# Performance work log

Hardware: AMD Instinct MI355X
Metric: run time of the kernel (lower is better)

Reference implementation:

```python
import jax, jax.numpy as jnp
import numpy as np
from jax import lax

B, C, N = 8, 3, 65536
NUM_POINTS = 1024


def setup_inputs() -> dict:
    key = jax.random.key(0)
    points = jax.random.normal(key, (B, C, N), dtype=jnp.float32)
    return {"points": points}


def furthest_point_sampling(xyz, num_points):
    # xyz: (B, N, 3) -> indices (B, num_points), int32
    b, n, _ = xyz.shape
    init_idx = jnp.zeros((b,), dtype=jnp.int32)  # CUDA FPS seeds with index 0
    init_dists = jnp.full((b, n), 1e10, dtype=xyz.dtype)

    def step(carry, _):
        dists, last_idx = carry
        last_pt = jnp.take_along_axis(xyz, last_idx[:, None, None], axis=1)  # (B,1,3)
        d = jnp.sum(jnp.square(xyz - last_pt), axis=-1)  # (B,N) squared dist to newest pt
        dists = jnp.minimum(dists, d)
        nxt = jnp.argmax(dists, axis=-1).astype(jnp.int32)
        return (dists, nxt), nxt

    (_, _), rest = lax.scan(step, (init_dists, init_idx), None, length=num_points - 1)
    # rest: (num_points-1, B) -> (B, num_points)
    idx = jnp.concatenate([init_idx[None, :], rest], axis=0).T
    return idx


def reference(points):
    # points: (B, 3, N), channels-first as in the torch module
    xyz = jnp.transpose(points, (0, 2, 1))  # (B, N, 3)
    idx = furthest_point_sampling(xyz, NUM_POINTS)  # (B, num_points)
    # fps_gather_by_index: gather along point axis of (B, 3, N)
    new_points = jnp.take_along_axis(points, idx[:, None, :], axis=2)  # (B, 3, num_points)
    return new_points
```

## Files before the change

kernel.cpp:

```cpp
#include <hip/hip_runtime.h>


namespace {

constexpr int kB = 8;
constexpr int kN = 65536;
constexpr int kNP = 1024;
constexpr int kPB = 16;
constexpr int kThreads = 256;
constexpr int kPPT = kN / (kPB * kThreads);
constexpr int kGrp = kPPT / 4;
constexpr int kWaves = kThreads / 64;
constexpr int kRgn = 16;

__device__ __forceinline__ unsigned long long shfl_xor_u64(unsigned long long v, int off) {
  return (unsigned long long)__shfl_xor((long long)v, off, 64);
}

__device__ __forceinline__ unsigned long long u64max(unsigned long long a,
                                                     unsigned long long b) {
  return a > b ? a : b;
}

__device__ __forceinline__ unsigned long long load_l2(const unsigned long long* p) {
  unsigned long long v;
  asm volatile("global_load_dwordx2 %0, %1, off sc0\n\ts_waitcnt vmcnt(0)"
               : "=v"(v)
               : "v"(p)
               : "memory");
  return v;
}

__device__ __forceinline__ void store_l2(unsigned long long* p, unsigned long long v) {
  asm volatile("global_store_dwordx2 %0, %1, off sc0" ::"v"(p), "v"(v) : "memory");
}

__global__ __launch_bounds__(kThreads) void fps_kernel(const float* __restrict__ pts,
                                                       float* __restrict__ out,
                                                       unsigned long long* __restrict__ slots) {
  const int batch = blockIdx.x & 7;
  const int slice = blockIdx.x >> 3;
  const int tid = threadIdx.x;
  const int lane = tid & 63;
  const int wave = tid >> 6;

  const float* __restrict__ xb = pts + (size_t)batch * 3 * kN;
  const float* __restrict__ yb = xb + kN;
  const float* __restrict__ zb = xb + 2 * kN;

  __shared__ unsigned long long s_wkey[kWaves];
  __shared__ unsigned s_win[2];
  __shared__ int s_hist[kNP];

  if (tid == 0) {
    s_win[0] = 0xFFFFFFFFu;
    s_win[1] = 0xFFFFFFFFu;
  }

  const int sbase = slice * (kThreads * kPPT);
  const int base0 = sbase + tid * 4;
  float px[kPPT], py[kPPT], pz[kPPT], dist[kPPT];
#pragma unroll
  for (int g = 0; g < kGrp; ++g) {
    const int base = base0 + g * (kThreads * 4);
    const float4 vx = *reinterpret_cast<const float4*>(xb + base);
    const float4 vy = *reinterpret_cast<const float4*>(yb + base);
    const float4 vz = *reinterpret_cast<const float4*>(zb + base);
    px[g * 4 + 0] = vx.x; px[g * 4 + 1] = vx.y; px[g * 4 + 2] = vx.z; px[g * 4 + 3] = vx.w;
    py[g * 4 + 0] = vy.x; py[g * 4 + 1] = vy.y; py[g * 4 + 2] = vy.z; py[g * 4 + 3] = vy.w;
    pz[g * 4 + 0] = vz.x; pz[g * 4 + 1] = vz.y; pz[g * 4 + 2] = vz.z; pz[g * 4 + 3] = vz.w;
  }
#pragma unroll
  for (int k = 0; k < kPPT; ++k) dist[k] = 1e10f;

  float qx = xb[0], qy = yb[0], qz = zb[0];

  unsigned long long* const sb = slots + (size_t)batch * kRgn * 32;

  for (int it = 1; it < kNP; ++it) {
    float bd = -1.0f;
    int bi = 0;
#pragma unroll
    for (int g = 0; g < kGrp; ++g) {
#pragma unroll
      for (int j = 0; j < 4; ++j) {
        const int k = g * 4 + j;
        const float dx = px[k] - qx;
        const float dy = py[k] - qy;
        const float dz = pz[k] - qz;
        const float ss =
            __fadd_rn(__fadd_rn(__fmul_rn(dx, dx), __fmul_rn(dy, dy)), __fmul_rn(dz, dz));
        const float nd = fminf(dist[k], ss);
        dist[k] = nd;
        if (nd > bd) {
          bd = nd;
          bi = base0 + g * (kThreads * 4) + j;
        }
      }
    }

    unsigned long long key = ((unsigned long long)__float_as_uint(bd) << 32) |
                             ((unsigned long long)(0xFFFFu - (unsigned)bi) << 16) |
                             (unsigned long long)(unsigned)it;

#pragma unroll
    for (int off = 32; off > 0; off >>= 1) {
      key = u64max(key, shfl_xor_u64(key, off));
    }
    if (lane == 0) s_wkey[wave] = key;
    __syncthreads();

    int wi;
    if (wave == 0) {
      unsigned long long bk = s_wkey[lane & (kWaves - 1)];
#pragma unroll
      for (int off = 1; off < kWaves; off <<= 1) {
        bk = u64max(bk, shfl_xor_u64(bk, off));
      }

      unsigned long long* const rgn = sb + (size_t)(it & (kRgn - 1)) * 32;
      if (lane == 0) {
        store_l2(rgn + slice, bk);
        __hip_atomic_store(rgn + 16 + slice, bk, __ATOMIC_RELAXED,
                           __HIP_MEMORY_SCOPE_AGENT);
      }

      unsigned long long w;
      int round = 0;
      for (;;) {
        unsigned long long a = load_l2(rgn + (lane & (kPB - 1)));
        bool ok = (unsigned)(a & 0xFFFFull) == (unsigned)it;
        if (round > 4 && (round & 1)) {
          const unsigned long long fb = __hip_atomic_load(
              rgn + 16 + (lane & (kPB - 1)), __ATOMIC_RELAXED, __HIP_MEMORY_SCOPE_AGENT);
          if (!ok && (unsigned)(fb & 0xFFFFull) == (unsigned)it) {
            a = fb;
            ok = true;
          }
        }
        if (__all(ok)) {
          w = a;
          break;
        }
        ++round;
      }
#pragma unroll
      for (int off = 1; off < kPB; off <<= 1) {
        w = u64max(w, shfl_xor_u64(w, off));
      }
      wi = (int)(0xFFFFu - ((unsigned)(w >> 16) & 0xFFFFu));
      if (lane == 0) {
        s_hist[it] = wi;
        __hip_atomic_store(&s_win[it & 1], ((unsigned)wi << 16) | (unsigned)it,
                           __ATOMIC_RELAXED, __HIP_MEMORY_SCOPE_WORKGROUP);
      }
    } else {
      unsigned v;
      do {
        v = __hip_atomic_load(&s_win[it & 1], __ATOMIC_RELAXED, __HIP_MEMORY_SCOPE_WORKGROUP);
      } while ((v & 0xFFFFu) != (unsigned)it);
      wi = (int)(v >> 16);
    }

    const int wiu = __builtin_amdgcn_readfirstlane(wi);
    qx = xb[wiu];
    qy = yb[wiu];
    qz = zb[wiu];
  }

  __syncthreads();

  if (slice == 0) {
    float* __restrict__ ob = out + (size_t)batch * 3 * kNP;
    for (int j = tid; j < kNP; j += kThreads) {
      const int id = (j == 0) ? 0 : s_hist[j];
      ob[j] = xb[id];
      ob[kNP + j] = yb[id];
      ob[2 * kNP + j] = zb[id];
    }
  }
}

}

extern "C" void kernel_launch(void* const* d_in, const int* in_sizes, int n_in,
                              void* d_out, int out_size, void* d_ws, size_t ws_size,
                              hipStream_t stream) {
  (void)in_sizes;
  (void)n_in;
  (void)out_size;
  (void)ws_size;
  const float* pts = (const float*)d_in[0];
  float* out = (float*)d_out;
  unsigned long long* slots = (unsigned long long*)d_ws;
  fps_kernel<<<dim3(kB * kPB), dim3(kThreads), 0, stream>>>(pts, out, slots);
}
```

Before: 1.768 ms.

## Place batch slices on same XCC and drop intra-block barrier from reduction

Blocks now read their XCC id and claim a batch slice through atomic counters, so each batch's 16 cooperating blocks tend to share one XCC and its L2, which should cut cross-die latency in the per-iteration exchange. The grid is oversized to 256 blocks; surplus blocks wait for all arrivals, then fill vacant slices or exit. Each wave now publishes its own key to global slots, removing the per-iteration __syncthreads, and wave 0 polls all 64 wave slots. The change adds a memset launch and startup atomics, and depends on every block being co-resident, which the spin-wait assumes.

```diff
diff --git a/kernel.cpp b/kernel.cpp
--- a/kernel.cpp
+++ b/kernel.cpp
@@ -11,7 +11,10 @@
 constexpr int kPPT = kN / (kPB * kThreads);
 constexpr int kGrp = kPPT / 4;
 constexpr int kWaves = kThreads / 64;
+constexpr int kSlots = kPB * kWaves;
 constexpr int kRgn = 16;
+constexpr int kRgnStride = 2 * kSlots;
+constexpr int kBlocks = 256;
 
 __device__ __forceinline__ unsigned long long shfl_xor_u64(unsigned long long v, int off) {
   return (unsigned long long)__shfl_xor((long long)v, off, 64);
@@ -37,25 +40,59 @@
 
 __global__ __launch_bounds__(kThreads) void fps_kernel(const float* __restrict__ pts,
                                                        float* __restrict__ out,
-                                                       unsigned long long* __restrict__ slots) {
-  const int batch = blockIdx.x & 7;
-  const int slice = blockIdx.x >> 3;
+                                                       unsigned long long* __restrict__ slots,
+                                                       unsigned* __restrict__ ctrl) {
   const int tid = threadIdx.x;
   const int lane = tid & 63;
   const int wave = tid >> 6;
 
+  __shared__ int s_batch, s_slice;
+  __shared__ unsigned s_win[2];
+  __shared__ int s_hist[kNP];
+
+  if (tid == 0) {
+    unsigned xcc;
+    asm volatile("s_getreg_b32 %0, hwreg(HW_REG_XCC_ID)" : "=s"(xcc));
+    const int home = (int)(xcc & 7u);
+    int batch = -1, slice = -1;
+    const int pos = (int)atomicAdd(&ctrl[home], 1u);
+    if (pos < kPB) {
+      batch = home;
+      slice = pos;
+    }
+    __hip_atomic_fetch_add(&ctrl[8], 1u, __ATOMIC_RELEASE, __HIP_MEMORY_SCOPE_AGENT);
+    if (batch < 0) {
+      while (__hip_atomic_load(&ctrl[8], __ATOMIC_ACQUIRE, __HIP_MEMORY_SCOPE_AGENT) <
+             (unsigned)kBlocks) {
+        __builtin_amdgcn_s_sleep(8);
+      }
+      int need = (int)atomicAdd(&ctrl[9], 1u);
+      for (int j = 0; j < kB; ++j) {
+        int have = (int)__hip_atomic_load(&ctrl[j], __ATOMIC_RELAXED, __HIP_MEMORY_SCOPE_AGENT);
+        have = have > kPB ? kPB : have;
+        const int vac = kPB - have;
+        if (need < vac) {
+          batch = j;
+          slice = have + need;
+          break;
+        }
+        need -= vac;
+      }
+    }
+    s_batch = batch;
+    s_slice = slice;
+    s_win[0] = 0xFFFFFFFFu;
+    s_win[1] = 0xFFFFFFFFu;
+  }
+  __syncthreads();
+
+  const int batch = s_batch;
+  const int slice = s_slice;
+  if (batch < 0) return;
+
   const float* __restrict__ xb = pts + (size_t)batch * 3 * kN;
   const float* __restrict__ yb = xb + kN;
   const float* __restrict__ zb = xb + 2 * kN;
-
-  __shared__ unsigned long long s_wkey[kWaves];
-  __shared__ unsigned s_win[2];
-  __shared__ int s_hist[kNP];
-
-  if (tid == 0) {
-    s_win[0] = 0xFFFFFFFFu;
-    s_win[1] = 0xFFFFFFFFu;
-  }
 
   const int sbase = slice * (kThreads * kPPT);
   const int base0 = sbase + tid * 4;
@@ -75,7 +112,8 @@
 
   float qx = xb[0], qy = yb[0], qz = zb[0];
 
-  unsigned long long* const sb = slots + (size_t)batch * kRgn * 32;
+  unsigned long long* const sb = slots + (size_t)batch * kRgn * kRgnStride;
+  const int wslot = slice * kWaves + wave;
 
   for (int it = 1; it < kNP; ++it) {
     float bd = -1.0f;
@@ -107,32 +145,23 @@
     for (int off = 32; off > 0; off >>= 1) {
       key = u64max(key, shfl_xor_u64(key, off));
     }
-    if (lane == 0) s_wkey[wave] = key;
-    __syncthreads();
+    unsigned long long* const rgn = sb + (size_t)(it & (kRgn - 1)) * kRgnStride;
+    if (lane == 0) {
+      store_l2(rgn + wslot, key);
+      __hip_atomic_store(rgn + kSlots + wslot, key, __ATOMIC_RELAXED,
+                         __HIP_MEMORY_SCOPE_AGENT);
+    }
 
     int wi;
     if (wave == 0) {
-      unsigned long long bk = s_wkey[lane & (kWaves - 1)];
-#pragma unroll
-      for (int off = 1; off < kWaves; off <<= 1) {
-        bk = u64max(bk, shfl_xor_u64(bk, off));
-      }
-
-      unsigned long long* const rgn = sb + (size_t)(it & (kRgn - 1)) * 32;
-      if (lane == 0) {
-        store_l2(rgn + slice, bk);
-        __hip_atomic_store(rgn + 16 + slice, bk, __ATOMIC_RELAXED,
-                           __HIP_MEMORY_SCOPE_AGENT);
-      }
-
       unsigned long long w;
       int round = 0;
       for (;;) {
-        unsigned long long a = load_l2(rgn + (lane & (kPB - 1)));
+        unsigned long long a = load_l2(rgn + lane);
         bool ok = (unsigned)(a & 0xFFFFull) == (unsigned)it;
-        if (round > 4 && (round & 1)) {
-          const unsigned long long fb = __hip_atomic_load(
-              rgn + 16 + (lane & (kPB - 1)), __ATOMIC_RELAXED, __HIP_MEMORY_SCOPE_AGENT);
+        if (round >= 3 && (round & 1)) {
+          const unsigned long long fb = __hip_atomic_load(rgn + kSlots + lane, __ATOMIC_RELAXED,
+                                                          __HIP_MEMORY_SCOPE_AGENT);
           if (!ok && (unsigned)(fb & 0xFFFFull) == (unsigned)it) {
             a = fb;
             ok = true;
@@ -145,7 +174,7 @@
         ++round;
       }
 #pragma unroll
-      for (int off = 1; off < kPB; off <<= 1) {
+      for (int off = 1; off < kSlots; off <<= 1) {
         w = u64max(w, shfl_xor_u64(w, off));
       }
       wi = (int)(0xFFFFu - ((unsigned)(w >> 16) & 0xFFFFu));
@@ -192,6 +221,8 @@
   (void)ws_size;
   const float* pts = (const float*)d_in[0];
   float* out = (float*)d_out;
-  unsigned long long* slots = (unsigned long long*)d_ws;
-  fps_kernel<<<dim3(kB * kPB), dim3(kThreads), 0, stream>>>(pts, out, slots);
-}
+  unsigned* ctrl = (unsigned*)d_ws;
+  unsigned long long* slots = (unsigned long long*)((char*)d_ws + 1024);
+  hipMemsetAsync(d_ws, 0, 256, stream);
+  fps_kernel<<<dim3(kBlocks), dim3(kThreads), 0, stream>>>(pts, out, slots, ctrl);
+}
```

New measurement: 2.068 ms. +17.0%, slower.
